# Optimization experiments

Measured on AMD Instinct MI355X. Metric: run time of the kernel, lower is better.

Reference implementation:

```python
import jax, jax.numpy as jnp
import numpy as np

DIM = 1024
HEADS = 16
DIM_HEAD = 64
INNER = HEADS * DIM_HEAD
B, N = 2, 2048


def rope_encoding(seq_len, dim_head):
    inv_freq = 1.0 / (10000.0 ** (jnp.arange(0, dim_head, 2, dtype=jnp.float32) / dim_head))
    pos = jnp.arange(seq_len, dtype=jnp.float32)
    sinusoid = pos[:, None] * inv_freq[None, :]          # [n, d/2]
    return jnp.concatenate([jnp.sin(sinusoid), jnp.cos(sinusoid)], axis=-1)  # [n, d]


def setup_inputs() -> dict:
    key = jax.random.key(0)
    k1, k2, k3, k4 = jax.random.split(key, 4)
    feats = jax.random.normal(k1, (B, N, DIM), dtype=jnp.float32)
    mask = jnp.ones((B, N), dtype=bool)
    # params (torch Linear: y = x @ W.T + b; store as [in, out] for x @ W)
    W_qkv = jax.random.normal(k2, (DIM, 3 * INNER), dtype=jnp.float32) / np.sqrt(DIM)
    W_out = jax.random.normal(k3, (INNER, DIM), dtype=jnp.float32) / np.sqrt(INNER)
    b_out = jax.random.normal(k4, (DIM,), dtype=jnp.float32) * 0.01
    return {"feats": feats, "W_qkv": W_qkv, "W_out": W_out, "b_out": b_out, "mask": mask}


def reference(feats, W_qkv, W_out, b_out, mask):
    b, n, _ = feats.shape
    h, d = HEADS, DIM_HEAD
    scale = d ** -0.5

    qkv = feats @ W_qkv                                   # [b, n, 3*inner]
    q, k, v = jnp.split(qkv, 3, axis=-1)
    to_bhnd = lambda t: t.reshape(b, n, h, d).transpose(0, 2, 1, 3)
    q, k, v = to_bhnd(q), to_bhnd(k), to_bhnd(v)          # [b, h, n, d]

    rope = rope_encoding(n, d)                            # [n, d]
    q = q + rope
    k = k + rope

    m = mask[:, None, :, None]                            # [b, 1, n, 1]
    neg_max = -jnp.finfo(k.dtype).max
    k = jnp.where(m, k, neg_max)

    q = jax.nn.softmax(q, axis=-1)                        # over feature dim
    k = jax.nn.softmax(k, axis=-2)                        # over sequence dim
    q = q * scale
    v = jnp.where(m, v, 0.0)

    context = jnp.einsum('bhnd,bhne->bhde', k, v)         # [b, h, d, d]
    out = jnp.einsum('bhde,bhnd->bhne', context, q)       # [b, h, n, d]
    out = out.transpose(0, 2, 1, 3).reshape(b, n, h * d)  # [b, n, inner]
    out = out @ W_out + b_out                             # [b, n, dim]

    attn = jnp.einsum('bhnd,bhmd->bhnm', q, k) * scale    # [b, h, n, n]
    return out, attn
```

## Files before the change

kernel.cpp:

```cpp
#include <hip/hip_runtime.h>
#include <cstddef>


#define BB     2
#define SEQ    2048
#define DIMM   1024
#define NHEADS 16
#define DH     64
#define TRIPLE 3072
#define ROWS   (BB*SEQ)
#define SCALE  0.125f

typedef unsigned short u16;
typedef unsigned int   u32;
typedef short s16x8 __attribute__((ext_vector_type(8)));
typedef float f32x4 __attribute__((ext_vector_type(4)));
typedef float vf4   __attribute__((ext_vector_type(4)));

static constexpr size_t WS_QB   = 0;
static constexpr size_t WS_KB   = 8388608;
static constexpr size_t WS_DEN  = 16777216;
static constexpr size_t WS_CTX  = WS_DEN + 8192;
static constexpr size_t WS_ROPE = WS_CTX + 524288;

static constexpr size_t SC_QKV  = 0;
static constexpr size_t SC_APK  = 50331648;
static constexpr size_t SC_WQPK = 67108864;
static constexpr size_t SC_WOPK = 79691776;
static constexpr size_t SC_OPF  = 83886080;
static constexpr size_t SC_OPPK = 100663296;

__device__ __forceinline__ u16 f2bf(float x) {
    u32 u = __float_as_uint(x);
    return (u16)((u + 0x7fffu + ((u >> 16) & 1u)) >> 16);
}
__device__ __forceinline__ float bf2f(u16 h) {
    return __uint_as_float(((u32)h) << 16);
}

__global__ __launch_bounds__(256) void zerok(float4* __restrict__ p)
{
    p[blockIdx.x * 256 + threadIdx.x] = float4{0.f, 0.f, 0.f, 0.f};
}

__global__ __launch_bounds__(256) void ropek(float* __restrict__ rope)
{
    int idx = blockIdx.x * 256 + threadIdx.x;
    int pos = idx >> 6;
    int d   = idx & 63;
    int i   = d & 31;
    double invf = pow(10000.0, -(double)i / 32.0);
    double a = (double)pos * invf;
    rope[idx] = (float)((d < 32) ? sin(a) : cos(a));
}

__global__ __launch_bounds__(256)
void conv_pack(const float* __restrict__ src, u16* __restrict__ dst)
{
    int t  = blockIdx.x * 256 + threadIdx.x;
    int g  = t & 3;
    int kb = (t >> 2) & 31;
    int row = t >> 7;
    const float* s = src + (size_t)row * 1024 + kb * 32 + 4 * g;
    float4 xa = *(const float4*)s;
    float4 xb = *(const float4*)(s + 16);
    float xs[8] = {xa.x, xa.y, xa.z, xa.w, xb.x, xb.y, xb.z, xb.w};
    s16x8 hv, lv;
    #pragma unroll
    for (int e = 0; e < 8; ++e) {
        u16 h = f2bf(xs[e]);
        hv[e] = (short)h;
        lv[e] = (short)f2bf(xs[e] - bf2f(h));
    }
    size_t rowc = (size_t)row * 256 + kb * 8;
    int sw = row & 7;
    *(s16x8*)(dst + (rowc + (size_t)(g ^ sw)) * 8)       = hv;
    *(s16x8*)(dst + (rowc + (size_t)((4 | g) ^ sw)) * 8) = lv;
}

__global__ __launch_bounds__(256)
void conv_packT(const float* __restrict__ W, u16* __restrict__ dst, int N)
{
    __shared__ float fb[32][128];
    int n0 = blockIdx.x * 128, k0 = blockIdx.y * 32, kb = blockIdx.y;
    int t = threadIdx.x;
    #pragma unroll
    for (int q = 0; q < 4; ++q) {
        int cc = q * 256 + t;
        int kr = cc >> 5, nc = (cc & 31) * 4;
        *(float4*)&fb[kr][nc] = *(const float4*)&W[(size_t)(k0 + kr) * N + n0 + nc];
    }
    __syncthreads();
    #pragma unroll
    for (int it = 0; it < 2; ++it) {
        int item = it * 256 + t;
        int g = (item >> 7) & 3, n = item & 127;
        s16x8 hv, lv;
        #pragma unroll
        for (int e = 0; e < 4; ++e) {
            float x0 = fb[4 * g + e][n];
            float x1 = fb[16 + 4 * g + e][n];
            u16 h0 = f2bf(x0), h1 = f2bf(x1);
            hv[e]     = (short)h0;
            hv[e + 4] = (short)h1;
            lv[e]     = (short)f2bf(x0 - bf2f(h0));
            lv[e + 4] = (short)f2bf(x1 - bf2f(h1));
        }
        int row = n0 + n;
        size_t rowc = (size_t)row * 256 + kb * 8;
        int sw = row & 7;
        *(s16x8*)(dst + (rowc + (size_t)(g ^ sw)) * 8)       = hv;
        *(s16x8*)(dst + (rowc + (size_t)((4 | g) ^ sw)) * 8) = lv;
    }
}

template<int MODE>
__global__ __launch_bounds__(256)
void gemm_split(const u16* __restrict__ Ap, const u16* __restrict__ Bp,
                float* __restrict__ C, int ldc, const float* __restrict__ bias,
                const float* __restrict__ rope, float* __restrict__ den)
{
    __shared__ __align__(16) char smem[65536];
    const int tid = threadIdx.x;
    const int lane = tid & 63, wid = tid >> 6;
    const int wi = wid >> 1, wj = wid & 1;
    const int r16 = lane & 15, g = lane >> 4;
    const int brow = blockIdx.y * 128, bcol = blockIdx.x * 128;

    const int srow = wid * 32 + (lane >> 3);
    const int sch  = lane & 7;
    const char* gA = (const char*)Ap + ((size_t)(brow + srow) * 256 + sch) * 16;
    const char* gB = (const char*)Bp + ((size_t)(bcol + srow) * 256 + sch) * 16;

    auto STAGE = [&](int buf, int kb) {
        size_t koff = (size_t)kb * 128;
        char* la = smem + buf * 32768 + wid * 4096;
        char* lb = smem + buf * 32768 + 16384 + wid * 4096;
        #pragma unroll
        for (int q = 0; q < 4; ++q) {
            __builtin_amdgcn_global_load_lds(
                (const __attribute__((address_space(1))) void*)(gA + (size_t)q * (8 * 4096) + koff),
                (__attribute__((address_space(3))) void*)(la + q * 1024), 16, 0, 0);
            __builtin_amdgcn_global_load_lds(
                (const __attribute__((address_space(1))) void*)(gB + (size_t)q * (8 * 4096) + koff),
                (__attribute__((address_space(3))) void*)(lb + q * 1024), 16, 0, 0);
        }
    };

    f32x4 acc[4][4] = {};
    STAGE(0, 0);
    __syncthreads();
    for (int kb = 0; kb < 32; ++kb) {
        const int cur = kb & 1;
        if (kb < 31) STAGE(cur ^ 1, kb + 1);

        const char* Ab = smem + cur * 32768;
        const char* Bb = smem + cur * 32768 + 16384;
        s16x8 ah[4], al[4], bh[4], bl[4];
        #pragma unroll
        for (int i = 0; i < 4; ++i) {
            int ra = wi * 64 + i * 16 + r16;
            const s16x8* Ar = (const s16x8*)(Ab + (size_t)ra * 128);
            ah[i] = Ar[g ^ (ra & 7)];
            al[i] = Ar[(4 | g) ^ (ra & 7)];
            int rb = wj * 64 + i * 16 + r16;
            const s16x8* Br = (const s16x8*)(Bb + (size_t)rb * 128);
            bh[i] = Br[g ^ (rb & 7)];
            bl[i] = Br[(4 | g) ^ (rb & 7)];
        }
        #pragma unroll
        for (int i = 0; i < 4; ++i)
            #pragma unroll
            for (int j = 0; j < 4; ++j) {
                acc[i][j] = __builtin_amdgcn_mfma_f32_16x16x32_bf16(ah[i], bh[j], acc[i][j], 0, 0, 0);
                acc[i][j] = __builtin_amdgcn_mfma_f32_16x16x32_bf16(ah[i], bl[j], acc[i][j], 0, 0, 0);
                acc[i][j] = __builtin_amdgcn_mfma_f32_16x16x32_bf16(al[i], bh[j], acc[i][j], 0, 0, 0);
            }
        __syncthreads();
    }

    if (MODE == 1) {
        #pragma unroll
        for (int i = 0; i < 4; ++i) {
            int row = brow + wi * 64 + i * 16 + g * 4;
            #pragma unroll
            for (int j = 0; j < 4; ++j) {
                int col = bcol + wj * 64 + j * 16 + r16;
                float bv = bias[col];
                #pragma unroll
                for (int r = 0; r < 4; ++r)
                    C[(size_t)(row + r) * ldc + col] = acc[i][j][r] + bv;
            }
        }
        return;
    }

    const int bx = blockIdx.x;
    if (bx < 16) {
        float* rl = (float*)smem;
        const int pos0 = brow & (SEQ - 1);
        #pragma unroll
        for (int q = 0; q < 8; ++q) {
            int u = q * 256 + tid;
            int rr = u >> 4, c4 = (u & 15) * 4;
            *(float4*)&rl[rr * 68 + c4] = *(const float4*)&rope[(size_t)(pos0 + rr) * 64 + c4];
        }
        __syncthreads();

        if (bx < 8) {
            #pragma unroll
            for (int i = 0; i < 4; ++i)
                #pragma unroll
                for (int r = 0; r < 4; ++r) {
                    int rloc = wi * 64 + i * 16 + g * 4 + r;
                    float v[4];
                    #pragma unroll
                    for (int j = 0; j < 4; ++j)
                        v[j] = acc[i][j][r] + rl[rloc * 68 + j * 16 + r16];
                    float m = fmaxf(fmaxf(v[0], v[1]), fmaxf(v[2], v[3]));
                    #pragma unroll
                    for (int o = 1; o <= 8; o <<= 1) m = fmaxf(m, __shfl_xor(m, o));
                    float e[4];
                    float s = 0.f;
                    #pragma unroll
                    for (int j = 0; j < 4; ++j) { e[j] = expf(v[j] - m); s += e[j]; }
                    #pragma unroll
                    for (int o = 1; o <= 8; o <<= 1) s += __shfl_xor(s, o);
                    float inv = SCALE / s;
                    size_t rb = (size_t)(brow + rloc) * ldc + bcol + wj * 64;
                    #pragma unroll
                    for (int j = 0; j < 4; ++j)
                        C[rb + j * 16 + r16] = e[j] * inv;
                }
        } else {
            float dsum[4] = {0.f, 0.f, 0.f, 0.f};
            #pragma unroll
            for (int i = 0; i < 4; ++i)
                #pragma unroll
                for (int r = 0; r < 4; ++r) {
                    int rloc = wi * 64 + i * 16 + g * 4 + r;
                    size_t rb = (size_t)(brow + rloc) * ldc + bcol + wj * 64;
                    #pragma unroll
                    for (int j = 0; j < 4; ++j) {
                        float e = expf(acc[i][j][r] + rl[rloc * 68 + j * 16 + r16]);
                        C[rb + j * 16 + r16] = e;
                        dsum[j] += e;
                    }
                }
            const int bD = (brow >> 11) * DIMM;
            #pragma unroll
            for (int j = 0; j < 4; ++j) {
                float s = dsum[j];
                s += __shfl_xor(s, 16);
                s += __shfl_xor(s, 32);
                if (g == 0)
                    atomicAdd(&den[bD + (bcol - DIMM) + wj * 64 + j * 16 + r16], s);
            }
        }
    } else {
        #pragma unroll
        for (int i = 0; i < 4; ++i) {
            int row = brow + wi * 64 + i * 16 + g * 4;
            #pragma unroll
            for (int j = 0; j < 4; ++j) {
                int col = bcol + wj * 64 + j * 16 + r16;
                #pragma unroll
                for (int r = 0; r < 4; ++r)
                    C[(size_t)(row + r) * ldc + col] = acc[i][j][r];
            }
        }
    }
}

__global__ __launch_bounds__(256)
void pack_qk(const float* __restrict__ qkv, const float* __restrict__ den,
             u16* __restrict__ qb, u16* __restrict__ kb)
{
    int t = blockIdx.x * 256 + threadIdx.x;
    int g  = t & 3;
    int db = (t >> 2) & 1;
    int h  = (t >> 3) & 15;
    int row = t >> 7;
    int b = row >> 11, n = row & (SEQ - 1);
    size_t dst = ((size_t)(b * NHEADS + h) * SEQ + n) * 64 + db * 32 + g * 8;
    const float* sq = qkv + (size_t)row * TRIPLE + h * DH + db * 32 + 4 * g;
    {
        float4 xa = *(const float4*)sq;
        float4 xb = *(const float4*)(sq + 16);
        float xs[8] = {xa.x, xa.y, xa.z, xa.w, xb.x, xb.y, xb.z, xb.w};
        s16x8 hv;
        #pragma unroll
        for (int e = 0; e < 8; ++e) hv[e] = (short)f2bf(xs[e]);
        *(s16x8*)(qb + dst) = hv;
    }
    {
        const float* sk = sq + DIMM;
        const float* dn = den + (size_t)b * DIMM + h * DH + db * 32 + 4 * g;
        float4 xa = *(const float4*)sk;
        float4 xb = *(const float4*)(sk + 16);
        float4 da = *(const float4*)dn;
        float4 dc = *(const float4*)(dn + 16);
        float xs[8] = {xa.x / da.x, xa.y / da.y, xa.z / da.z, xa.w / da.w,
                       xb.x / dc.x, xb.y / dc.y, xb.z / dc.z, xb.w / dc.w};
        s16x8 hv;
        #pragma unroll
        for (int e = 0; e < 8; ++e) hv[e] = (short)f2bf(xs[e]);
        *(s16x8*)(kb + dst) = hv;
    }
}

__global__ __launch_bounds__(256)
void contextk(const float* __restrict__ qkv, const float* __restrict__ den,
              float* __restrict__ ctx)
{
    int chunk = blockIdx.x;
    int h = blockIdx.y, b = blockIdx.z;
    int row0 = b * SEQ + chunk * 256;
    __shared__ float kt[32][64];
    __shared__ float vt[32][64];
    int d  = threadIdx.x & 63;
    int eg = threadIdx.x >> 6;
    float acc[16] = {};
    for (int t = 0; t < 8; ++t) {
        #pragma unroll
        for (int q = 0; q < 2; ++q) {
            int lf = threadIdx.x * 2 + q;
            int nn = lf >> 4;
            int c4 = (lf & 15) * 4;
            size_t base = (size_t)(row0 + t * 32 + nn) * TRIPLE + DIMM + h * DH + c4;
            *reinterpret_cast<float4*>(&kt[nn][c4]) = *reinterpret_cast<const float4*>(&qkv[base]);
            *reinterpret_cast<float4*>(&vt[nn][c4]) = *reinterpret_cast<const float4*>(&qkv[base + DIMM]);
        }
        __syncthreads();
        #pragma unroll 8
        for (int nn = 0; nn < 32; ++nn) {
            float kv = kt[nn][d];
            #pragma unroll
            for (int j = 0; j < 16; ++j)
                acc[j] = fmaf(kv, vt[nn][eg * 16 + j], acc[j]);
        }
        __syncthreads();
    }
    float rden = 1.f / den[(size_t)b * DIMM + h * DH + d];
    size_t cb = ((size_t)(b * NHEADS + h)) * (DH * DH) + d * DH + eg * 16;
    #pragma unroll
    for (int j = 0; j < 16; ++j) atomicAdd(&ctx[cb + j], acc[j] * rden);
}

__global__ __launch_bounds__(256)
void outpre(const float* __restrict__ qkv, const float* __restrict__ ctx,
            float* __restrict__ op)
{
    int h = blockIdx.y, b = blockIdx.z;
    int row0 = b * SEQ + blockIdx.x * 64;
    __shared__ float cl[64][64];
    __shared__ float ql[4][64];
    const float* C = ctx + ((size_t)(b * NHEADS + h)) * (DH * DH);
    for (int i = threadIdx.x; i < DH * DH; i += 256) cl[i >> 6][i & 63] = C[i];
    __syncthreads();
    int w = threadIdx.x >> 6, lane = threadIdx.x & 63;
    for (int it = 0; it < 16; ++it) {
        int row = row0 + w * 16 + it;
        float qv = qkv[(size_t)row * TRIPLE + h * DH + lane];
        ql[w][lane] = qv;
        float acc = 0.f;
        #pragma unroll
        for (int d = 0; d < 64; ++d) acc = fmaf(cl[d][lane], ql[w][d], acc);
        op[(size_t)row * DIMM + h * DH + lane] = acc;
    }
}

__global__ __launch_bounds__(256)
void attnk(const u16* __restrict__ qb, const u16* __restrict__ kb, float* __restrict__ attn)
{
    __shared__ float ost[16384];
    int bh = blockIdx.z;
    int n0 = blockIdx.y * 128, m0 = blockIdx.x * 128;
    int tid = threadIdx.x, lane = tid & 63, wid = tid >> 6;
    int wi = wid >> 1, wj = wid & 1;
    int r16 = lane & 15, g = lane >> 4;
    const u16* qB = qb + (size_t)bh * (SEQ * 64);
    const u16* kB = kb + (size_t)bh * (SEQ * 64);
    f32x4 acc[4][4] = {};
    #pragma unroll
    for (int db = 0; db < 2; ++db) {
        s16x8 a[4], b[4];
        #pragma unroll
        for (int i = 0; i < 4; ++i) {
            a[i] = *(const s16x8*)(qB + (size_t)(n0 + wi * 64 + i * 16 + r16) * 64 + db * 32 + g * 8);
            b[i] = *(const s16x8*)(kB + (size_t)(m0 + wj * 64 + i * 16 + r16) * 64 + db * 32 + g * 8);
        }
        #pragma unroll
        for (int i = 0; i < 4; ++i)
            #pragma unroll
            for (int j = 0; j < 4; ++j)
                acc[i][j] = __builtin_amdgcn_mfma_f32_16x16x32_bf16(a[i], b[j], acc[i][j], 0, 0, 0);
    }
    #pragma unroll
    for (int i = 0; i < 4; ++i)
        #pragma unroll
        for (int j = 0; j < 4; ++j)
            #pragma unroll
            for (int r = 0; r < 4; ++r)
                ost[(wi * 64 + i * 16 + g * 4 + r) * 128 + wj * 64 + j * 16 + r16] =
                    acc[i][j][r] * SCALE;
    __syncthreads();
    size_t base = (size_t)bh * ((size_t)SEQ * SEQ) + (size_t)n0 * SEQ + m0;
    int rr = tid >> 5, c16 = tid & 31;
    #pragma unroll
    for (int it = 0; it < 16; ++it) {
        int row = rr * 16 + it;
        vf4 v = *(vf4*)&ost[row * 128 + c16 * 4];
        __builtin_nontemporal_store(v, (vf4*)&attn[base + (size_t)row * SEQ + c16 * 4]);
    }
}

extern "C" void kernel_launch(void* const* d_in, const int* in_sizes, int n_in,
                              void* d_out, int out_size, void* d_ws, size_t ws_size,
                              hipStream_t stream)
{
    const float* feats = (const float*)d_in[0];
    const float* Wqkv  = (const float*)d_in[1];
    const float* Wout  = (const float*)d_in[2];
    const float* bout  = (const float*)d_in[3];

    char*  wsb  = (char*)d_ws;
    u16*   qb   = (u16*)(wsb + WS_QB);
    u16*   kb   = (u16*)(wsb + WS_KB);
    float* den  = (float*)(wsb + WS_DEN);
    float* rope = (float*)(wsb + WS_ROPE);
    float* ctx  = (float*)(wsb + WS_CTX);

    float* out  = (float*)d_out;
    float* attn = out + (size_t)ROWS * DIMM;
    char*  sc   = (char*)attn;
    float* qkv    = (float*)(sc + SC_QKV);
    u16*   A_pk   = (u16*)(sc + SC_APK);
    u16*   Wq_pk  = (u16*)(sc + SC_WQPK);
    u16*   Wo_pk  = (u16*)(sc + SC_WOPK);
    float* op_f   = (float*)(sc + SC_OPF);
    u16*   Op_pk  = (u16*)(sc + SC_OPPK);

    zerok<<<130, 256, 0, stream>>>(reinterpret_cast<float4*>(den));
    ropek<<<512, 256, 0, stream>>>(rope);
    conv_pack<<<2048, 256, 0, stream>>>(feats, A_pk);
    conv_packT<<<dim3(24, 32), 256, 0, stream>>>(Wqkv, Wq_pk, TRIPLE);
    conv_packT<<<dim3(8, 32), 256, 0, stream>>>(Wout, Wo_pk, DIMM);
    gemm_split<0><<<dim3(24, 32), 256, 0, stream>>>(A_pk, Wq_pk, qkv, TRIPLE,
                                                    nullptr, rope, den);
    pack_qk<<<2048, 256, 0, stream>>>(qkv, den, qb, kb);
    contextk<<<dim3(8, NHEADS, BB), 256, 0, stream>>>(qkv, den, ctx);
    outpre<<<dim3(SEQ / 64, NHEADS, BB), 256, 0, stream>>>(qkv, ctx, op_f);
    conv_pack<<<2048, 256, 0, stream>>>(op_f, Op_pk);
    gemm_split<1><<<dim3(8, 32), 256, 0, stream>>>(Op_pk, Wo_pk, out, DIMM,
                                                   bout, nullptr, nullptr);
    attnk<<<dim3(16, 16, 32), 256, 0, stream>>>(qb, kb, attn);
}
```

Before: 358.7 us.

## Fuse bf16 split packing into outpre, swizzle GEMM blocks, single-buffer QKV GEMM

The outpre kernel now writes the hi/lo bf16-split, swizzled packed layout directly, so the intermediate fp32 buffer and the separate conv_pack launch go away. Both GEMMs switch to a 1D grid with an XCD-aware block swizzle meant to improve L2 locality. The QKV GEMM drops double buffering to a single 36 KB LDS buffer so three blocks can reside per CU, trading load/compute overlap for occupancy. The fused packing uses scattered 2-byte stores, which may write less efficiently than the old vectorized pack.

```diff
diff --git a/kernel.cpp b/kernel.cpp
--- a/kernel.cpp
+++ b/kernel.cpp
@@ -27,7 +27,6 @@
 static constexpr size_t SC_APK  = 50331648;
 static constexpr size_t SC_WQPK = 67108864;
 static constexpr size_t SC_WOPK = 79691776;
-static constexpr size_t SC_OPF  = 83886080;
 static constexpr size_t SC_OPPK = 100663296;
 
 __device__ __forceinline__ u16 f2bf(float x) {
@@ -115,27 +114,32 @@
 }
 
 template<int MODE>
-__global__ __launch_bounds__(256)
+__global__ __launch_bounds__(256, MODE == 0 ? 3 : 2)
 void gemm_split(const u16* __restrict__ Ap, const u16* __restrict__ Bp,
                 float* __restrict__ C, int ldc, const float* __restrict__ bias,
                 const float* __restrict__ rope, float* __restrict__ den)
 {
-    __shared__ __align__(16) char smem[65536];
+    constexpr int SMEM_BYTES = (MODE == 0) ? 36864 : 65536;
+    __shared__ __align__(16) char smem[SMEM_BYTES];
     const int tid = threadIdx.x;
     const int lane = tid & 63, wid = tid >> 6;
     const int wi = wid >> 1, wj = wid & 1;
     const int r16 = lane & 15, g = lane >> 4;
-    const int brow = blockIdx.y * 128, bcol = blockIdx.x * 128;
+
+    constexpr int NX  = (MODE == 0) ? 24 : 8;
+    constexpr int CPX = (MODE == 0) ? 96 : 32;
+    const int bid = blockIdx.x;
+    const int swz = (bid & 7) * CPX + (bid >> 3);
+    const int bx = swz % NX, by = swz / NX;
+    const int brow = by * 128, bcol = bx * 128;
 
     const int srow = wid * 32 + (lane >> 3);
     const int sch  = lane & 7;
     const char* gA = (const char*)Ap + ((size_t)(brow + srow) * 256 + sch) * 16;
     const char* gB = (const char*)Bp + ((size_t)(bcol + srow) * 256 + sch) * 16;
 
-    auto STAGE = [&](int buf, int kb) {
+    auto STAGE = [&](char* la, char* lb, int kb) {
         size_t koff = (size_t)kb * 128;
-        char* la = smem + buf * 32768 + wid * 4096;
-        char* lb = smem + buf * 32768 + 16384 + wid * 4096;
         #pragma unroll
         for (int q = 0; q < 4; ++q) {
             __builtin_amdgcn_global_load_lds(
@@ -146,16 +150,7 @@
                 (__attribute__((address_space(3))) void*)(lb + q * 1024), 16, 0, 0);
         }
     };
-
-    f32x4 acc[4][4] = {};
-    STAGE(0, 0);
-    __syncthreads();
-    for (int kb = 0; kb < 32; ++kb) {
-        const int cur = kb & 1;
-        if (kb < 31) STAGE(cur ^ 1, kb + 1);
-
-        const char* Ab = smem + cur * 32768;
-        const char* Bb = smem + cur * 32768 + 16384;
+    auto COMPUTE = [&](const char* Ab, const char* Bb, f32x4 (&acc)[4][4]) {
         s16x8 ah[4], al[4], bh[4], bl[4];
         #pragma unroll
         for (int i = 0; i < 4; ++i) {
@@ -176,7 +171,29 @@
                 acc[i][j] = __builtin_amdgcn_mfma_f32_16x16x32_bf16(ah[i], bl[j], acc[i][j], 0, 0, 0);
                 acc[i][j] = __builtin_amdgcn_mfma_f32_16x16x32_bf16(al[i], bh[j], acc[i][j], 0, 0, 0);
             }
+    };
+
+    f32x4 acc[4][4] = {};
+    if constexpr (MODE == 0) {
+        char* la = smem + wid * 4096;
+        char* lb = smem + 16384 + wid * 4096;
+        for (int kb = 0; kb < 32; ++kb) {
+            STAGE(la, lb, kb);
+            __syncthreads();
+            COMPUTE(smem, smem + 16384, acc);
+            __syncthreads();
+        }
+    } else {
+        STAGE(smem + wid * 4096, smem + 16384 + wid * 4096, 0);
         __syncthreads();
+        for (int kb = 0; kb < 32; ++kb) {
+            const int cur = kb & 1;
+            if (kb < 31)
+                STAGE(smem + (cur ^ 1) * 32768 + wid * 4096,
+                      smem + (cur ^ 1) * 32768 + 16384 + wid * 4096, kb + 1);
+            COMPUTE(smem + cur * 32768, smem + cur * 32768 + 16384, acc);
+            __syncthreads();
+        }
     }
 
     if (MODE == 1) {
@@ -195,7 +212,6 @@
         return;
     }
 
-    const int bx = blockIdx.x;
     if (bx < 16) {
         float* rl = (float*)smem;
         const int pos0 = brow & (SEQ - 1);
@@ -349,7 +365,7 @@
 
 __global__ __launch_bounds__(256)
 void outpre(const float* __restrict__ qkv, const float* __restrict__ ctx,
-            float* __restrict__ op)
+            u16* __restrict__ op_pk)
 {
     int h = blockIdx.y, b = blockIdx.z;
     int row0 = b * SEQ + blockIdx.x * 64;
@@ -359,6 +375,10 @@
     for (int i = threadIdx.x; i < DH * DH; i += 256) cl[i >> 6][i & 63] = C[i];
     __syncthreads();
     int w = threadIdx.x >> 6, lane = threadIdx.x & 63;
+    const int m    = lane & 31;
+    const int kbI  = h * 2 + (lane >> 5);
+    const int g2   = (m & 15) >> 2;
+    const int elem = (m & 3) | ((m >> 4) << 2);
     for (int it = 0; it < 16; ++it) {
         int row = row0 + w * 16 + it;
         float qv = qkv[(size_t)row * TRIPLE + h * DH + lane];
@@ -366,7 +386,12 @@
         float acc = 0.f;
         #pragma unroll
         for (int d = 0; d < 64; ++d) acc = fmaf(cl[d][lane], ql[w][d], acc);
-        op[(size_t)row * DIMM + h * DH + lane] = acc;
+        u16 hi = f2bf(acc);
+        u16 lo = f2bf(acc - bf2f(hi));
+        int sw = row & 7;
+        size_t base = (size_t)row * 2048 + (size_t)kbI * 64;
+        op_pk[base + ((g2 ^ sw) * 8 + elem)]       = hi;
+        op_pk[base + (((4 | g2) ^ sw) * 8 + elem)] = lo;
     }
 }
 
@@ -438,7 +463,6 @@
     u16*   A_pk   = (u16*)(sc + SC_APK);
     u16*   Wq_pk  = (u16*)(sc + SC_WQPK);
     u16*   Wo_pk  = (u16*)(sc + SC_WOPK);
-    float* op_f   = (float*)(sc + SC_OPF);
     u16*   Op_pk  = (u16*)(sc + SC_OPPK);
 
     zerok<<<130, 256, 0, stream>>>(reinterpret_cast<float4*>(den));
@@ -446,13 +470,12 @@
     conv_pack<<<2048, 256, 0, stream>>>(feats, A_pk);
     conv_packT<<<dim3(24, 32), 256, 0, stream>>>(Wqkv, Wq_pk, TRIPLE);
     conv_packT<<<dim3(8, 32), 256, 0, stream>>>(Wout, Wo_pk, DIMM);
-    gemm_split<0><<<dim3(24, 32), 256, 0, stream>>>(A_pk, Wq_pk, qkv, TRIPLE,
-                                                    nullptr, rope, den);
+    gemm_split<0><<<768, 256, 0, stream>>>(A_pk, Wq_pk, qkv, TRIPLE,
+                                           nullptr, rope, den);
     pack_qk<<<2048, 256, 0, stream>>>(qkv, den, qb, kb);
     contextk<<<dim3(8, NHEADS, BB), 256, 0, stream>>>(qkv, den, ctx);
-    outpre<<<dim3(SEQ / 64, NHEADS, BB), 256, 0, stream>>>(qkv, ctx, op_f);
-    conv_pack<<<2048, 256, 0, stream>>>(op_f, Op_pk);
-    gemm_split<1><<<dim3(8, 32), 256, 0, stream>>>(Op_pk, Wo_pk, out, DIMM,
-                                                   bout, nullptr, nullptr);
+    outpre<<<dim3(SEQ / 64, NHEADS, BB), 256, 0, stream>>>(qkv, ctx, Op_pk);
+    gemm_split<1><<<256, 256, 0, stream>>>(Op_pk, Wo_pk, out, DIMM,
+                                           bout, nullptr, nullptr);
     attnk<<<dim3(16, 16, 32), 256, 0, stream>>>(qb, kb, attn);
 }
```

After: 343.5 us. 1.04x faster.
